# Kernel tuning notes

Measured on AMD Instinct MI355X. Metric: run time of the kernel, lower is better.

The kernel has to match this reference:

```python
import jax, jax.numpy as jnp
import numpy as np

# Forest of complete binary trees modeling query plans.
B = 512          # number of plans (trees)
D = 11           # tree depth; leaves at level D-1
LEAVES = 1 << (D - 1)      # 1024 leaves per tree
N_INT = LEAVES - 1         # 1023 internal nodes per tree (BFS heap order)
F_LEAF = 64      # leaf ('Scan') feature dim
F_INT = 32       # internal operator feature dim
H = 128          # hidden_dim
NHID = 4         # num_layers=5 -> input layer + 4 hidden layers
DV = 32          # data_vec_dim
OUT = 1 + DV     # latency + data vector


def _mlp(x, W_in, b_in, W_hid, b_hid, W_out, b_out):
    """GenericUnit: Linear+ReLU input layer, NHID Linear+ReLU hidden layers, linear output."""
    h = jax.nn.relu(x @ W_in + b_in)
    for i in range(W_hid.shape[0]):  # small fixed loop over layers
        h = jax.nn.relu(h @ W_hid[i] + b_hid[i])
    return h @ W_out + b_out


def setup_inputs() -> dict:
    key = jax.random.key(0)
    ks = jax.random.split(key, 8)

    def w(k, shape, fan_in):
        return jax.random.normal(k, shape, jnp.float32) * np.float32(1.0 / np.sqrt(fan_in))

    return {
        "leaf_feat": jax.random.normal(ks[0], (B, LEAVES, F_LEAF), jnp.float32),
        "int_feat": jax.random.normal(ks[1], (B, N_INT, F_INT), jnp.float32),
        # leaf unit (0 children)
        "leaf_W_in": w(ks[2], (F_LEAF, H), F_LEAF),
        "leaf_b_in": jnp.zeros((H,), jnp.float32),
        "leaf_W_hid": w(ks[3], (NHID, H, H), H),
        "leaf_b_hid": jnp.zeros((NHID, H), jnp.float32),
        "leaf_W_out": w(ks[4], (H, OUT), H),
        "leaf_b_out": jnp.zeros((OUT,), jnp.float32),
        # internal unit (2 children): input = F_INT + 2*OUT = 98
        "int_W_in": w(ks[5], (F_INT + 2 * OUT, H), F_INT + 2 * OUT),
        "int_b_in": jnp.zeros((H,), jnp.float32),
        "int_W_hid": w(ks[6], (NHID, H, H), H),
        "int_b_hid": jnp.zeros((NHID, H), jnp.float32),
        "int_W_out": w(ks[7], (H, OUT), H),
        "int_b_out": jnp.zeros((OUT,), jnp.float32),
    }


def reference(leaf_feat, int_feat,
              leaf_W_in, leaf_b_in, leaf_W_hid, leaf_b_hid, leaf_W_out, leaf_b_out,
              int_W_in, int_b_in, int_W_hid, int_b_hid, int_W_out, int_b_out):
    # Leaves (level D-1): [B, LEAVES, OUT]
    cur = _mlp(leaf_feat, leaf_W_in, leaf_b_in, leaf_W_hid, leaf_b_hid, leaf_W_out, leaf_b_out)
    # Bottom-up over internal levels; level d has 2^d nodes at BFS offsets [2^d-1, 2^(d+1)-1)
    for d in range(D - 2, -1, -1):
        n = 1 << d
        feats = int_feat[:, n - 1: 2 * n - 1, :]            # [B, n, F_INT]
        children = cur.reshape(B, n, 2 * OUT)               # concat of two child outputs
        unit_in = jnp.concatenate([feats, children], axis=-1)
        cur = _mlp(unit_in, int_W_in, int_b_in, int_W_hid, int_b_hid, int_W_out, int_b_out)
    # Root output, latency channel: [B]
    return cur[:, 0, 0]
```

## Files before the change

kernel.cpp:

```cpp
#include <hip/hip_runtime.h>
#include <cstdint>
#include <cstddef>

constexpr int Bn     = 512;
constexpr int Dd     = 11;
constexpr int LEAVES = 1024;
constexpr int NINT   = 1023;
constexpr int FLEAF  = 64;
constexpr int FINT   = 32;
constexpr int Hh     = 128;
constexpr int OUTC   = 33;

#define THREADS 256
constexpr int KSTR  = 136;
constexpr int MATSZ = 128 * KSTR;

using short8 = __attribute__((ext_vector_type(8))) short;
using f32x4  = __attribute__((ext_vector_type(4))) float;

__device__ __forceinline__ unsigned int f2bf_rne_u(float f) {
  unsigned int u = __float_as_uint(f);
  u += 0x7fffu + ((u >> 16) & 1);
  return u;
}
__device__ __forceinline__ unsigned short f2bf_rne(float f) {
  return (unsigned short)(f2bf_rne_u(f) >> 16);
}
__device__ __forceinline__ float bf2f(unsigned short h) {
  return __uint_as_float((unsigned int)h << 16);
}
__device__ __forceinline__ float trunc_bf(float a) {
  return __uint_as_float(__float_as_uint(a) & 0xffff0000u);
}
__device__ __forceinline__ unsigned int pack_hi_trunc(float a, float b) {
  return (__float_as_uint(a) >> 16) | (__float_as_uint(b) & 0xffff0000u);
}
__device__ __forceinline__ unsigned int pack_lo_rne(float a, float b) {
  return (f2bf_rne_u(a) >> 16) | (f2bf_rne_u(b) & 0xffff0000u);
}

template <int KC, int MT>
__device__ __forceinline__ void dense_layer(
    unsigned short* Ah, unsigned short* Al,
    const unsigned short* __restrict__ WTh, const unsigned short* __restrict__ WTl,
    const float* __restrict__ bias)
{
  const int tid  = threadIdx.x;
  const int wave = tid >> 6;
  const int lane = tid & 63;
  const int quad = lane >> 4;
  const int l16  = lane & 15;
  const int nbase = wave * 32;

  short8 wh[2][KC];
#pragma unroll
  for (int nt = 0; nt < 2; ++nt) {
    const int n = nbase + nt * 16 + l16;
#pragma unroll
    for (int kc = 0; kc < KC; ++kc)
      wh[nt][kc] = *(const short8*)&WTh[n * KSTR + kc * 32 + quad * 8];
  }
  float4 bv[2];
#pragma unroll
  for (int nt = 0; nt < 2; ++nt)
    bv[nt] = *(const float4*)&bias[nbase + nt * 16 + quad * 4];

  f32x4 c[MT][2];
#pragma unroll
  for (int mt = 0; mt < MT; ++mt)
#pragma unroll
    for (int nt = 0; nt < 2; ++nt) c[mt][nt] = (f32x4){0.f, 0.f, 0.f, 0.f};

#pragma unroll
  for (int kc = 0; kc < KC; ++kc) {
    const int k0 = kc * 32 + quad * 8;
    short8 wl[2];
#pragma unroll
    for (int nt = 0; nt < 2; ++nt) {
      const int n = nbase + nt * 16 + l16;
      wl[nt] = *(const short8*)&WTl[n * KSTR + k0];
    }
    short8 ah[MT], al[MT];
#pragma unroll
    for (int mt = 0; mt < MT; ++mt) {
      ah[mt] = *(const short8*)&Ah[(mt * 16 + l16) * KSTR + k0];
      al[mt] = *(const short8*)&Al[(mt * 16 + l16) * KSTR + k0];
    }
#pragma unroll
    for (int mt = 0; mt < MT; ++mt)
#pragma unroll
      for (int nt = 0; nt < 2; ++nt)
        c[mt][nt] = __builtin_amdgcn_mfma_f32_16x16x32_bf16(wh[nt][kc], ah[mt], c[mt][nt], 0, 0, 0);
#pragma unroll
    for (int mt = 0; mt < MT; ++mt)
#pragma unroll
      for (int nt = 0; nt < 2; ++nt)
        c[mt][nt] = __builtin_amdgcn_mfma_f32_16x16x32_bf16(wh[nt][kc], al[mt], c[mt][nt], 0, 0, 0);
#pragma unroll
    for (int mt = 0; mt < MT; ++mt)
#pragma unroll
      for (int nt = 0; nt < 2; ++nt)
        c[mt][nt] = __builtin_amdgcn_mfma_f32_16x16x32_bf16(wl[nt], ah[mt], c[mt][nt], 0, 0, 0);
  }
  __syncthreads();

#pragma unroll
  for (int mt = 0; mt < MT; ++mt) {
    const int m = mt * 16 + l16;
#pragma unroll
    for (int nt = 0; nt < 2; ++nt) {
      const int nb = nbase + nt * 16 + quad * 4;
      float v0 = fmaxf(c[mt][nt][0] + bv[nt].x, 0.f);
      float v1 = fmaxf(c[mt][nt][1] + bv[nt].y, 0.f);
      float v2 = fmaxf(c[mt][nt][2] + bv[nt].z, 0.f);
      float v3 = fmaxf(c[mt][nt][3] + bv[nt].w, 0.f);
      const unsigned int h0 = pack_hi_trunc(v0, v1);
      const unsigned int h1 = pack_hi_trunc(v2, v3);
      const unsigned int l0 = pack_lo_rne(v0 - trunc_bf(v0), v1 - trunc_bf(v1));
      const unsigned int l1 = pack_lo_rne(v2 - trunc_bf(v2), v3 - trunc_bf(v3));
      *(uint2*)&Ah[m * KSTR + nb] = make_uint2(h0, h1);
      *(uint2*)&Al[m * KSTR + nb] = make_uint2(l0, l1);
    }
  }
  __syncthreads();
}

template <int MT>
__device__ __forceinline__ void out_layer(
    const unsigned short* Ah, const unsigned short* Al,
    const unsigned short* __restrict__ WTh, const unsigned short* __restrict__ WTl,
    const float* __restrict__ bias,
    unsigned short* outH, unsigned short* outL, float* finalOut)
{
  const int tid  = threadIdx.x;
  const int wave = tid >> 6;
  const int lane = tid & 63;
  const int quad = lane >> 4;
  const int l16  = lane & 15;
  if (wave < 3) {
    const int n_row = wave * 16 + l16;
    short8 wh[4], wl[4];
#pragma unroll
    for (int kc = 0; kc < 4; ++kc) {
      wh[kc] = *(const short8*)&WTh[n_row * KSTR + kc * 32 + quad * 8];
      wl[kc] = *(const short8*)&WTl[n_row * KSTR + kc * 32 + quad * 8];
    }
    const int nb = wave * 16 + quad * 4;
    const float4 bv = *(const float4*)&bias[nb];
    const float bvr[4] = {bv.x, bv.y, bv.z, bv.w};

    f32x4 c[MT];
#pragma unroll
    for (int mt = 0; mt < MT; ++mt) c[mt] = (f32x4){0.f, 0.f, 0.f, 0.f};
#pragma unroll
    for (int kc = 0; kc < 4; ++kc) {
      const int k0 = kc * 32 + quad * 8;
#pragma unroll
      for (int mt = 0; mt < MT; ++mt) {
        const short8 ah = *(const short8*)&Ah[(mt * 16 + l16) * KSTR + k0];
        const short8 al = *(const short8*)&Al[(mt * 16 + l16) * KSTR + k0];
        c[mt] = __builtin_amdgcn_mfma_f32_16x16x32_bf16(wh[kc], ah, c[mt], 0, 0, 0);
        c[mt] = __builtin_amdgcn_mfma_f32_16x16x32_bf16(wh[kc], al, c[mt], 0, 0, 0);
        c[mt] = __builtin_amdgcn_mfma_f32_16x16x32_bf16(wl[kc], ah, c[mt], 0, 0, 0);
      }
    }
#pragma unroll
    for (int mt = 0; mt < MT; ++mt) {
      const int m = mt * 16 + l16;
#pragma unroll
      for (int r = 0; r < 4; ++r) {
        const int n = nb + r;
        const float v = c[mt][r] + bvr[r];
        if (n < OUTC) {
          outH[m * 33 + n] = (unsigned short)(__float_as_uint(v) >> 16);
          outL[m * 33 + n] = f2bf_rne(v - trunc_bf(v));
        }
        if (finalOut && n == 0 && m == 0) *finalOut = v;
      }
    }
  }
}

__global__ __launch_bounds__(THREADS, 4)
void leaf_kernel(const float* __restrict__ X,
                 const unsigned short* __restrict__ warena,
                 const float* __restrict__ barena,
                 unsigned short* __restrict__ outH, unsigned short* __restrict__ outL)
{
  __shared__ unsigned short Ah[64 * KSTR];
  __shared__ unsigned short Al[64 * KSTR];
  const int row_base = blockIdx.x * 64;
  const int tid = threadIdx.x;

  for (int e = tid; e < 64 * 16; e += THREADS) {
    const int r  = e >> 4;
    const int k0 = (e & 15) << 2;
    const float4 v = *(const float4*)&X[(size_t)(row_base + r) * FLEAF + k0];
    const unsigned int h0 = pack_hi_trunc(v.x, v.y);
    const unsigned int h1 = pack_hi_trunc(v.z, v.w);
    const unsigned int l0 = pack_lo_rne(v.x - trunc_bf(v.x), v.y - trunc_bf(v.y));
    const unsigned int l1 = pack_lo_rne(v.z - trunc_bf(v.z), v.w - trunc_bf(v.w));
    *(uint2*)&Ah[r * KSTR + k0] = make_uint2(h0, h1);
    *(uint2*)&Al[r * KSTR + k0] = make_uint2(l0, l1);
  }
  __syncthreads();

  dense_layer<2, 4>(Ah, Al, warena + 0 * 2 * MATSZ, warena + 0 * 2 * MATSZ + MATSZ, barena + 0 * 128);
#pragma unroll
  for (int l = 0; l < 4; ++l) {
    const int id = 1 + l;
    dense_layer<4, 4>(Ah, Al, warena + id * 2 * MATSZ, warena + id * 2 * MATSZ + MATSZ, barena + id * 128);
  }
  out_layer<4>(Ah, Al, warena + 5 * 2 * MATSZ, warena + 5 * 2 * MATSZ + MATSZ, barena + 5 * 128,
               outH + (size_t)row_base * 33, outL + (size_t)row_base * 33, nullptr);
}

__global__ __launch_bounds__(THREADS, 4)
void int_kernel(const float* __restrict__ feat,
                const unsigned short* __restrict__ prevH, const unsigned short* __restrict__ prevL,
                const unsigned short* __restrict__ warena, const float* __restrict__ barena,
                unsigned short* __restrict__ outH, unsigned short* __restrict__ outL,
                int n, int logn)
{
  __shared__ unsigned short Ah[64 * KSTR];
  __shared__ unsigned short Al[64 * KSTR];
  const int tid = threadIdx.x;
  const int m = tid & 63;
  const int g = tid >> 6;
  const int row = blockIdx.x * 64 + m;
  const int b = row >> logn;
  const int i = row & (n - 1);

  const float* fr = feat + ((size_t)b * NINT + (n - 1) + i) * FINT;
#pragma unroll
  for (int j = 0; j < 4; ++j) {
    const int cch = g + 4 * j;
    const float2 v = *(const float2*)&fr[cch * 2];
    *(unsigned int*)&Ah[m * KSTR + cch * 2] = pack_hi_trunc(v.x, v.y);
    *(unsigned int*)&Al[m * KSTR + cch * 2] = pack_lo_rne(v.x - trunc_bf(v.x), v.y - trunc_bf(v.y));
  }
  const size_t c0 = ((size_t)b * (n << 1) + (i << 1)) * 33;
#pragma unroll
  for (int j = 0; j < 9; ++j) {
    const int p = g + 4 * j;
    if (p < 33) {
      const unsigned int hv = *(const unsigned int*)&prevH[c0 + 2 * p];
      const unsigned int lv = *(const unsigned int*)&prevL[c0 + 2 * p];
      *(unsigned int*)&Ah[m * KSTR + 32 + 2 * p] = hv;
      *(unsigned int*)&Al[m * KSTR + 32 + 2 * p] = lv;
    }
  }
#pragma unroll
  for (int j = 0; j < 4; ++j) {
    const int p = g + 4 * j;
    if (p < 15) {
      *(unsigned int*)&Ah[m * KSTR + 98 + 2 * p] = 0u;
      *(unsigned int*)&Al[m * KSTR + 98 + 2 * p] = 0u;
    }
  }
  __syncthreads();

  dense_layer<4, 4>(Ah, Al, warena + 6 * 2 * MATSZ, warena + 6 * 2 * MATSZ + MATSZ, barena + 6 * 128);
#pragma unroll
  for (int l = 0; l < 4; ++l) {
    const int id = 7 + l;
    dense_layer<4, 4>(Ah, Al, warena + id * 2 * MATSZ, warena + id * 2 * MATSZ + MATSZ, barena + id * 128);
  }
  out_layer<4>(Ah, Al, warena + 11 * 2 * MATSZ, warena + 11 * 2 * MATSZ + MATSZ, barena + 11 * 128,
               outH + (size_t)blockIdx.x * 64 * 33, outL + (size_t)blockIdx.x * 64 * 33, nullptr);
}

__global__ __launch_bounds__(THREADS, 4)
void tail_kernel(const float* __restrict__ feat,
                 const unsigned short* __restrict__ g6H, const unsigned short* __restrict__ g6L,
                 const unsigned short* __restrict__ warena, const float* __restrict__ barena,
                 float* __restrict__ out)
{
  __shared__ unsigned short Ah[64 * KSTR];
  __shared__ unsigned short Al[64 * KSTR];
  __shared__ unsigned short oH[64 * 33];
  __shared__ unsigned short oL[64 * 33];
  const int tid = threadIdx.x;
  const int m = tid & 63;
  const int g = tid >> 6;
  const int b = blockIdx.x;

  for (int d = 5; d >= 0; --d) {
    const int n = 1 << d;
    const int i = m & (n - 1);
    const float* fr = feat + ((size_t)b * NINT + (n - 1) + i) * FINT;
#pragma unroll
    for (int j = 0; j < 4; ++j) {
      const int cch = g + 4 * j;
      const float2 v = *(const float2*)&fr[cch * 2];
      *(unsigned int*)&Ah[m * KSTR + cch * 2] = pack_hi_trunc(v.x, v.y);
      *(unsigned int*)&Al[m * KSTR + cch * 2] = pack_lo_rne(v.x - trunc_bf(v.x), v.y - trunc_bf(v.y));
    }
    const unsigned short* sH;
    const unsigned short* sL;
    size_t c0;
    if (d == 5) { sH = g6H; sL = g6L; c0 = ((size_t)b * 64 + 2 * i) * 33; }
    else        { sH = oH;  sL = oL;  c0 = (size_t)(2 * i) * 33; }
#pragma unroll
    for (int j = 0; j < 9; ++j) {
      const int p = g + 4 * j;
      if (p < 33) {
        const unsigned int hv = *(const unsigned int*)&sH[c0 + 2 * p];
        const unsigned int lv = *(const unsigned int*)&sL[c0 + 2 * p];
        *(unsigned int*)&Ah[m * KSTR + 32 + 2 * p] = hv;
        *(unsigned int*)&Al[m * KSTR + 32 + 2 * p] = lv;
      }
    }
#pragma unroll
    for (int j = 0; j < 4; ++j) {
      const int p = g + 4 * j;
      if (p < 15) {
        *(unsigned int*)&Ah[m * KSTR + 98 + 2 * p] = 0u;
        *(unsigned int*)&Al[m * KSTR + 98 + 2 * p] = 0u;
      }
    }
    __syncthreads();

    if (d == 5) {
      dense_layer<4, 2>(Ah, Al, warena + 6 * 2 * MATSZ, warena + 6 * 2 * MATSZ + MATSZ, barena + 6 * 128);
#pragma unroll
      for (int l = 0; l < 4; ++l) {
        const int id = 7 + l;
        dense_layer<4, 2>(Ah, Al, warena + id * 2 * MATSZ, warena + id * 2 * MATSZ + MATSZ, barena + id * 128);
      }
      out_layer<2>(Ah, Al, warena + 11 * 2 * MATSZ, warena + 11 * 2 * MATSZ + MATSZ, barena + 11 * 128,
                   oH, oL, nullptr);
    } else {
      dense_layer<4, 1>(Ah, Al, warena + 6 * 2 * MATSZ, warena + 6 * 2 * MATSZ + MATSZ, barena + 6 * 128);
#pragma unroll
      for (int l = 0; l < 4; ++l) {
        const int id = 7 + l;
        dense_layer<4, 1>(Ah, Al, warena + id * 2 * MATSZ, warena + id * 2 * MATSZ + MATSZ, barena + id * 128);
      }
      out_layer<1>(Ah, Al, warena + 11 * 2 * MATSZ, warena + 11 * 2 * MATSZ + MATSZ, barena + 11 * 128,
                   oH, oL, (d == 0) ? (out + b) : nullptr);
    }
    __syncthreads();
  }
}

__global__ void prep_kernel(const float* __restrict__ lW_in, const float* __restrict__ lW_hid,
                            const float* __restrict__ lW_out, const float* __restrict__ lb_in,
                            const float* __restrict__ lb_hid, const float* __restrict__ lb_out,
                            const float* __restrict__ iW_in, const float* __restrict__ iW_hid,
                            const float* __restrict__ iW_out, const float* __restrict__ ib_in,
                            const float* __restrict__ ib_hid, const float* __restrict__ ib_out,
                            unsigned short* __restrict__ warena, float* __restrict__ barena)
{
  const int id = blockIdx.y;
  const float* W; const float* bs; int K, N;
  if (id == 0)       { W = lW_in;                        bs = lb_in;                 K = FLEAF; N = Hh; }
  else if (id <= 4)  { W = lW_hid + (id - 1) * Hh * Hh;  bs = lb_hid + (id - 1) * Hh; K = Hh;   N = Hh; }
  else if (id == 5)  { W = lW_out;                       bs = lb_out;                K = Hh;    N = OUTC; }
  else if (id == 6)  { W = iW_in;                        bs = ib_in;                 K = FINT + 2 * OUTC; N = Hh; }
  else if (id <= 10) { W = iW_hid + (id - 7) * Hh * Hh;  bs = ib_hid + (id - 7) * Hh; K = Hh;   N = Hh; }
  else               { W = iW_out;                       bs = ib_out;                K = Hh;    N = OUTC; }

  unsigned short* dh = warena + id * 2 * MATSZ;
  unsigned short* dl = dh + MATSZ;
  const int e = blockIdx.x * THREADS + threadIdx.x;
  if (e < MATSZ) {
    const int nn = e / KSTR;
    const int kk = e - nn * KSTR;
    const float v = (kk < K && nn < N) ? W[(size_t)kk * N + nn] : 0.f;
    const unsigned short h = f2bf_rne(v);
    dh[e] = h;
    dl[e] = f2bf_rne(v - bf2f(h));
  }
  if (blockIdx.x == 0 && threadIdx.x < 128)
    barena[id * 128 + threadIdx.x] = (threadIdx.x < N) ? bs[threadIdx.x] : 0.f;
}

extern "C" void kernel_launch(void* const* d_in, const int* in_sizes, int n_in,
                              void* d_out, int out_size, void* d_ws, size_t ws_size,
                              hipStream_t stream) {
  const float* leaf_feat = (const float*)d_in[0];
  const float* int_feat  = (const float*)d_in[1];
  const float* lW_in  = (const float*)d_in[2];
  const float* lb_in  = (const float*)d_in[3];
  const float* lW_hid = (const float*)d_in[4];
  const float* lb_hid = (const float*)d_in[5];
  const float* lW_out = (const float*)d_in[6];
  const float* lb_out = (const float*)d_in[7];
  const float* iW_in  = (const float*)d_in[8];
  const float* ib_in  = (const float*)d_in[9];
  const float* iW_hid = (const float*)d_in[10];
  const float* ib_hid = (const float*)d_in[11];
  const float* iW_out = (const float*)d_in[12];
  const float* ib_out = (const float*)d_in[13];
  float* out = (float*)d_out;

  const size_t rowsA = (size_t)Bn * LEAVES;
  const size_t rowsB = rowsA / 2;
  unsigned short* AH = (unsigned short*)d_ws;
  unsigned short* AL = AH + rowsA * 33;
  unsigned short* BH = AL + rowsA * 33;
  unsigned short* BL = BH + rowsB * 33;
  unsigned short* warena = BL + rowsB * 33;
  float* barena = (float*)(warena + 24 * MATSZ);

  prep_kernel<<<dim3((MATSZ + THREADS - 1) / THREADS, 12), THREADS, 0, stream>>>(
      lW_in, lW_hid, lW_out, lb_in, lb_hid, lb_out,
      iW_in, iW_hid, iW_out, ib_in, ib_hid, ib_out, warena, barena);

  leaf_kernel<<<(Bn * LEAVES) / 64, THREADS, 0, stream>>>(leaf_feat, warena, barena, AH, AL);

  int_kernel<<<4096, THREADS, 0, stream>>>(int_feat, AH, AL, warena, barena, BH, BL, 512, 9);
  int_kernel<<<2048, THREADS, 0, stream>>>(int_feat, BH, BL, warena, barena, AH, AL, 256, 8);
  int_kernel<<<1024, THREADS, 0, stream>>>(int_feat, AH, AL, warena, barena, BH, BL, 128, 7);
  int_kernel<<< 512, THREADS, 0, stream>>>(int_feat, BH, BL, warena, barena, AH, AL,  64, 6);

  tail_kernel<<<Bn, THREADS, 0, stream>>>(int_feat, AH, AL, warena, barena, out);
}
```

Before: 930.7 us.

## Preload low weights, double-buffer LDS activation reads, coalesce int-kernel input staging

The dense and output layers now load all low-part weight fragments into registers up front and double-buffer the high-part activation fragments from LDS, so the next k-chunk's reads overlap the current MFMAs, with s_setprio raised around the MFMA blocks. The int kernel's staging of features and child outputs is reorganised into contiguous, coalesced float4 and uint loads across the whole block instead of per-row strided reads. The low-part bf16 packing uses the hardware v_cvt_pk_bf16_f32 instruction. Launch-bounds occupancy drops from 4 to 3 blocks per CU to make room for the extra registers, which may reduce latency hiding.

```diff
diff --git a/kernel.cpp b/kernel.cpp
--- a/kernel.cpp
+++ b/kernel.cpp
@@ -36,7 +36,9 @@
   return (__float_as_uint(a) >> 16) | (__float_as_uint(b) & 0xffff0000u);
 }
 __device__ __forceinline__ unsigned int pack_lo_rne(float a, float b) {
-  return (f2bf_rne_u(a) >> 16) | (f2bf_rne_u(b) & 0xffff0000u);
+  unsigned int r;
+  asm("v_cvt_pk_bf16_f32 %0, %1, %2" : "=v"(r) : "v"(a), "v"(b));
+  return r;
 }
 
 template <int KC, int MT>
@@ -52,57 +54,66 @@
   const int l16  = lane & 15;
   const int nbase = wave * 32;
 
-  short8 wh[2][KC];
+  short8 wh[2][KC], wl[2][KC];
 #pragma unroll
   for (int nt = 0; nt < 2; ++nt) {
     const int n = nbase + nt * 16 + l16;
 #pragma unroll
-    for (int kc = 0; kc < KC; ++kc)
+    for (int kc = 0; kc < KC; ++kc) {
       wh[nt][kc] = *(const short8*)&WTh[n * KSTR + kc * 32 + quad * 8];
-  }
+      wl[nt][kc] = *(const short8*)&WTl[n * KSTR + kc * 32 + quad * 8];
+    }
+  }
+
+  f32x4 c[MT][2];
+#pragma unroll
+  for (int mt = 0; mt < MT; ++mt)
+#pragma unroll
+    for (int nt = 0; nt < 2; ++nt) c[mt][nt] = (f32x4){0.f, 0.f, 0.f, 0.f};
+
+  short8 ah[2][MT];
+  short8 al[MT];
+#pragma unroll
+  for (int mt = 0; mt < MT; ++mt)
+    ah[0][mt] = *(const short8*)&Ah[(mt * 16 + l16) * KSTR + quad * 8];
+
+#pragma unroll
+  for (int kc = 0; kc < KC; ++kc) {
+    const int cur = kc & 1;
+    const int k0  = kc * 32 + quad * 8;
+#pragma unroll
+    for (int mt = 0; mt < MT; ++mt)
+      al[mt] = *(const short8*)&Al[(mt * 16 + l16) * KSTR + k0];
+    if (kc + 1 < KC) {
+      const int k1 = k0 + 32;
+#pragma unroll
+      for (int mt = 0; mt < MT; ++mt)
+        ah[cur ^ 1][mt] = *(const short8*)&Ah[(mt * 16 + l16) * KSTR + k1];
+    }
+    __builtin_amdgcn_s_setprio(1);
+#pragma unroll
+    for (int mt = 0; mt < MT; ++mt)
+#pragma unroll
+      for (int nt = 0; nt < 2; ++nt)
+        c[mt][nt] = __builtin_amdgcn_mfma_f32_16x16x32_bf16(wh[nt][kc], ah[cur][mt], c[mt][nt], 0, 0, 0);
+#pragma unroll
+    for (int mt = 0; mt < MT; ++mt)
+#pragma unroll
+      for (int nt = 0; nt < 2; ++nt)
+        c[mt][nt] = __builtin_amdgcn_mfma_f32_16x16x32_bf16(wl[nt][kc], ah[cur][mt], c[mt][nt], 0, 0, 0);
+#pragma unroll
+    for (int mt = 0; mt < MT; ++mt)
+#pragma unroll
+      for (int nt = 0; nt < 2; ++nt)
+        c[mt][nt] = __builtin_amdgcn_mfma_f32_16x16x32_bf16(wh[nt][kc], al[mt], c[mt][nt], 0, 0, 0);
+    __builtin_amdgcn_s_setprio(0);
+  }
+  __syncthreads();
+
   float4 bv[2];
 #pragma unroll
   for (int nt = 0; nt < 2; ++nt)
     bv[nt] = *(const float4*)&bias[nbase + nt * 16 + quad * 4];
-
-  f32x4 c[MT][2];
-#pragma unroll
-  for (int mt = 0; mt < MT; ++mt)
-#pragma unroll
-    for (int nt = 0; nt < 2; ++nt) c[mt][nt] = (f32x4){0.f, 0.f, 0.f, 0.f};
-
-#pragma unroll
-  for (int kc = 0; kc < KC; ++kc) {
-    const int k0 = kc * 32 + quad * 8;
-    short8 wl[2];
-#pragma unroll
-    for (int nt = 0; nt < 2; ++nt) {
-      const int n = nbase + nt * 16 + l16;
-      wl[nt] = *(const short8*)&WTl[n * KSTR + k0];
-    }
-    short8 ah[MT], al[MT];
-#pragma unroll
-    for (int mt = 0; mt < MT; ++mt) {
-      ah[mt] = *(const short8*)&Ah[(mt * 16 + l16) * KSTR + k0];
-      al[mt] = *(const short8*)&Al[(mt * 16 + l16) * KSTR + k0];
-    }
-#pragma unroll
-    for (int mt = 0; mt < MT; ++mt)
-#pragma unroll
-      for (int nt = 0; nt < 2; ++nt)
-        c[mt][nt] = __builtin_amdgcn_mfma_f32_16x16x32_bf16(wh[nt][kc], ah[mt], c[mt][nt], 0, 0, 0);
-#pragma unroll
-    for (int mt = 0; mt < MT; ++mt)
-#pragma unroll
-      for (int nt = 0; nt < 2; ++nt)
-        c[mt][nt] = __builtin_amdgcn_mfma_f32_16x16x32_bf16(wh[nt][kc], al[mt], c[mt][nt], 0, 0, 0);
-#pragma unroll
-    for (int mt = 0; mt < MT; ++mt)
-#pragma unroll
-      for (int nt = 0; nt < 2; ++nt)
-        c[mt][nt] = __builtin_amdgcn_mfma_f32_16x16x32_bf16(wl[nt], ah[mt], c[mt][nt], 0, 0, 0);
-  }
-  __syncthreads();
 
 #pragma unroll
   for (int mt = 0; mt < MT; ++mt) {
@@ -152,17 +163,34 @@
     f32x4 c[MT];
 #pragma unroll
     for (int mt = 0; mt < MT; ++mt) c[mt] = (f32x4){0.f, 0.f, 0.f, 0.f};
+
+    short8 ah[2][MT];
+    short8 al[MT];
+#pragma unroll
+    for (int mt = 0; mt < MT; ++mt)
+      ah[0][mt] = *(const short8*)&Ah[(mt * 16 + l16) * KSTR + quad * 8];
+
 #pragma unroll
     for (int kc = 0; kc < 4; ++kc) {
-      const int k0 = kc * 32 + quad * 8;
+      const int cur = kc & 1;
+      const int k0  = kc * 32 + quad * 8;
+#pragma unroll
+      for (int mt = 0; mt < MT; ++mt)
+        al[mt] = *(const short8*)&Al[(mt * 16 + l16) * KSTR + k0];
+      if (kc + 1 < 4) {
+        const int k1 = k0 + 32;
+#pragma unroll
+        for (int mt = 0; mt < MT; ++mt)
+          ah[cur ^ 1][mt] = *(const short8*)&Ah[(mt * 16 + l16) * KSTR + k1];
+      }
+      __builtin_amdgcn_s_setprio(1);
 #pragma unroll
       for (int mt = 0; mt < MT; ++mt) {
-        const short8 ah = *(const short8*)&Ah[(mt * 16 + l16) * KSTR + k0];
-        const short8 al = *(const short8*)&Al[(mt * 16 + l16) * KSTR + k0];
-        c[mt] = __builtin_amdgcn_mfma_f32_16x16x32_bf16(wh[kc], ah, c[mt], 0, 0, 0);
-        c[mt] = __builtin_amdgcn_mfma_f32_16x16x32_bf16(wh[kc], al, c[mt], 0, 0, 0);
-        c[mt] = __builtin_amdgcn_mfma_f32_16x16x32_bf16(wl[kc], ah, c[mt], 0, 0, 0);
-      }
+        c[mt] = __builtin_amdgcn_mfma_f32_16x16x32_bf16(wh[kc], ah[cur][mt], c[mt], 0, 0, 0);
+        c[mt] = __builtin_amdgcn_mfma_f32_16x16x32_bf16(wl[kc], ah[cur][mt], c[mt], 0, 0, 0);
+        c[mt] = __builtin_amdgcn_mfma_f32_16x16x32_bf16(wh[kc], al[mt], c[mt], 0, 0, 0);
+      }
+      __builtin_amdgcn_s_setprio(0);
     }
 #pragma unroll
     for (int mt = 0; mt < MT; ++mt) {
@@ -181,7 +209,7 @@
   }
 }
 
-__global__ __launch_bounds__(THREADS, 4)
+__global__ __launch_bounds__(THREADS, 3)
 void leaf_kernel(const float* __restrict__ X,
                  const unsigned short* __restrict__ warena,
                  const float* __restrict__ barena,
@@ -215,7 +243,7 @@
                outH + (size_t)row_base * 33, outL + (size_t)row_base * 33, nullptr);
 }
 
-__global__ __launch_bounds__(THREADS, 4)
+__global__ __launch_bounds__(THREADS, 3)
 void int_kernel(const float* __restrict__ feat,
                 const unsigned short* __restrict__ prevH, const unsigned short* __restrict__ prevL,
                 const unsigned short* __restrict__ warena, const float* __restrict__ barena,
@@ -224,32 +252,40 @@
 {
   __shared__ unsigned short Ah[64 * KSTR];
   __shared__ unsigned short Al[64 * KSTR];
-  const int tid = threadIdx.x;
+  const int tid  = threadIdx.x;
+  const int row0 = blockIdx.x * 64;
+  const int b    = row0 >> logn;
+  const int i0   = row0 & (n - 1);
+
+  const float* fr0 = feat + ((size_t)b * NINT + (n - 1) + i0) * FINT;
+#pragma unroll
+  for (int j = 0; j < 2; ++j) {
+    const int e  = tid + j * 256;
+    const int r  = e >> 3;
+    const int cc = (e & 7) << 2;
+    const float4 v = *(const float4*)&fr0[(size_t)e << 2];
+    const unsigned int h0 = pack_hi_trunc(v.x, v.y);
+    const unsigned int h1 = pack_hi_trunc(v.z, v.w);
+    const unsigned int l0 = pack_lo_rne(v.x - trunc_bf(v.x), v.y - trunc_bf(v.y));
+    const unsigned int l1 = pack_lo_rne(v.z - trunc_bf(v.z), v.w - trunc_bf(v.w));
+    *(uint2*)&Ah[r * KSTR + cc] = make_uint2(h0, h1);
+    *(uint2*)&Al[r * KSTR + cc] = make_uint2(l0, l1);
+  }
+  const size_t cbase = ((size_t)b * (n << 1) + (size_t)(i0 << 1)) * 33;
+  const unsigned int* srcH = (const unsigned int*)(prevH + cbase);
+  const unsigned int* srcL = (const unsigned int*)(prevL + cbase);
+#pragma unroll
+  for (int j = 0; j < 9; ++j) {
+    const int idx = tid + j * 256;
+    if (idx < 2112) {
+      const unsigned int mm = (unsigned int)idx / 33u;
+      const unsigned int pp = (unsigned int)idx - mm * 33u;
+      *(unsigned int*)&Ah[mm * KSTR + 32 + 2 * pp] = srcH[idx];
+      *(unsigned int*)&Al[mm * KSTR + 32 + 2 * pp] = srcL[idx];
+    }
+  }
   const int m = tid & 63;
   const int g = tid >> 6;
-  const int row = blockIdx.x * 64 + m;
-  const int b = row >> logn;
-  const int i = row & (n - 1);
-
-  const float* fr = feat + ((size_t)b * NINT + (n - 1) + i) * FINT;
-#pragma unroll
-  for (int j = 0; j < 4; ++j) {
-    const int cch = g + 4 * j;
-    const float2 v = *(const float2*)&fr[cch * 2];
-    *(unsigned int*)&Ah[m * KSTR + cch * 2] = pack_hi_trunc(v.x, v.y);
-    *(unsigned int*)&Al[m * KSTR + cch * 2] = pack_lo_rne(v.x - trunc_bf(v.x), v.y - trunc_bf(v.y));
-  }
-  const size_t c0 = ((size_t)b * (n << 1) + (i << 1)) * 33;
-#pragma unroll
-  for (int j = 0; j < 9; ++j) {
-    const int p = g + 4 * j;
-    if (p < 33) {
-      const unsigned int hv = *(const unsigned int*)&prevH[c0 + 2 * p];
-      const unsigned int lv = *(const unsigned int*)&prevL[c0 + 2 * p];
-      *(unsigned int*)&Ah[m * KSTR + 32 + 2 * p] = hv;
-      *(unsigned int*)&Al[m * KSTR + 32 + 2 * p] = lv;
-    }
-  }
 #pragma unroll
   for (int j = 0; j < 4; ++j) {
     const int p = g + 4 * j;
@@ -270,7 +306,7 @@
                outH + (size_t)blockIdx.x * 64 * 33, outL + (size_t)blockIdx.x * 64 * 33, nullptr);
 }
 
-__global__ __launch_bounds__(THREADS, 4)
+__global__ __launch_bounds__(THREADS, 3)
 void tail_kernel(const float* __restrict__ feat,
                  const unsigned short* __restrict__ g6H, const unsigned short* __restrict__ g6L,
                  const unsigned short* __restrict__ warena, const float* __restrict__ barena,
```

Measured after the change: 973.7 us. +4.6%, slower.

## Replace fused tail kernel with per-level int_kernel launches and hardware bf16 pack

Applied to the files above, without the earlier changes.

Removes the tail kernel, which had one block per tree walk levels 5..0 in sequence with rows padded to 16 or 32. Those six levels now go through the same int_kernel launched once per level with row-dense 64-row blocks. The root latency is written from the last launch through a per-row finalOut pointer. The low-half bf16 pack now uses the v_cvt_pk_bf16_f32 instruction instead of manual round-to-nearest-even bit arithmetic. In exchange the top levels need six extra small launches, and the smallest grids leave most CUs idle.

```diff
diff --git a/kernel.cpp b/kernel.cpp
--- a/kernel.cpp
+++ b/kernel.cpp
@@ -36,7 +36,9 @@
   return (__float_as_uint(a) >> 16) | (__float_as_uint(b) & 0xffff0000u);
 }
 __device__ __forceinline__ unsigned int pack_lo_rne(float a, float b) {
-  return (f2bf_rne_u(a) >> 16) | (f2bf_rne_u(b) & 0xffff0000u);
+  unsigned int r;
+  asm("v_cvt_pk_bf16_f32 %0, %1, %2" : "=v"(r) : "v"(a), "v"(b));
+  return r;
 }
 
 template <int KC, int MT>
@@ -175,7 +177,7 @@
           outH[m * 33 + n] = (unsigned short)(__float_as_uint(v) >> 16);
           outL[m * 33 + n] = f2bf_rne(v - trunc_bf(v));
         }
-        if (finalOut && n == 0 && m == 0) *finalOut = v;
+        if (finalOut && n == 0) finalOut[m] = v;
       }
     }
   }
@@ -220,6 +222,7 @@
                 const unsigned short* __restrict__ prevH, const unsigned short* __restrict__ prevL,
                 const unsigned short* __restrict__ warena, const float* __restrict__ barena,
                 unsigned short* __restrict__ outH, unsigned short* __restrict__ outL,
+                float* __restrict__ finalOut,
                 int n, int logn)
 {
   __shared__ unsigned short Ah[64 * KSTR];
@@ -267,81 +270,8 @@
     dense_layer<4, 4>(Ah, Al, warena + id * 2 * MATSZ, warena + id * 2 * MATSZ + MATSZ, barena + id * 128);
   }
   out_layer<4>(Ah, Al, warena + 11 * 2 * MATSZ, warena + 11 * 2 * MATSZ + MATSZ, barena + 11 * 128,
-               outH + (size_t)blockIdx.x * 64 * 33, outL + (size_t)blockIdx.x * 64 * 33, nullptr);
-}
-
-__global__ __launch_bounds__(THREADS, 4)
-void tail_kernel(const float* __restrict__ feat,
-                 const unsigned short* __restrict__ g6H, const unsigned short* __restrict__ g6L,
-                 const unsigned short* __restrict__ warena, const float* __restrict__ barena,
-                 float* __restrict__ out)
-{
-  __shared__ unsigned short Ah[64 * KSTR];
-  __shared__ unsigned short Al[64 * KSTR];
-  __shared__ unsigned short oH[64 * 33];
-  __shared__ unsigned short oL[64 * 33];
-  const int tid = threadIdx.x;
-  const int m = tid & 63;
-  const int g = tid >> 6;
-  const int b = blockIdx.x;
-
-  for (int d = 5; d >= 0; --d) {
-    const int n = 1 << d;
-    const int i = m & (n - 1);
-    const float* fr = feat + ((size_t)b * NINT + (n - 1) + i) * FINT;
-#pragma unroll
-    for (int j = 0; j < 4; ++j) {
-      const int cch = g + 4 * j;
-      const float2 v = *(const float2*)&fr[cch * 2];
-      *(unsigned int*)&Ah[m * KSTR + cch * 2] = pack_hi_trunc(v.x, v.y);
-      *(unsigned int*)&Al[m * KSTR + cch * 2] = pack_lo_rne(v.x - trunc_bf(v.x), v.y - trunc_bf(v.y));
-    }
-    const unsigned short* sH;
-    const unsigned short* sL;
-    size_t c0;
-    if (d == 5) { sH = g6H; sL = g6L; c0 = ((size_t)b * 64 + 2 * i) * 33; }
-    else        { sH = oH;  sL = oL;  c0 = (size_t)(2 * i) * 33; }
-#pragma unroll
-    for (int j = 0; j < 9; ++j) {
-      const int p = g + 4 * j;
-      if (p < 33) {
-        const unsigned int hv = *(const unsigned int*)&sH[c0 + 2 * p];
-        const unsigned int lv = *(const unsigned int*)&sL[c0 + 2 * p];
-        *(unsigned int*)&Ah[m * KSTR + 32 + 2 * p] = hv;
-        *(unsigned int*)&Al[m * KSTR + 32 + 2 * p] = lv;
-      }
-    }
-#pragma unroll
-    for (int j = 0; j < 4; ++j) {
-      const int p = g + 4 * j;
-      if (p < 15) {
-        *(unsigned int*)&Ah[m * KSTR + 98 + 2 * p] = 0u;
-        *(unsigned int*)&Al[m * KSTR + 98 + 2 * p] = 0u;
-      }
-    }
-    __syncthreads();
-
-    if (d == 5) {
-      dense_layer<4, 2>(Ah, Al, warena + 6 * 2 * MATSZ, warena + 6 * 2 * MATSZ + MATSZ, barena + 6 * 128);
-#pragma unroll
-      for (int l = 0; l < 4; ++l) {
-        const int id = 7 + l;
-        dense_layer<4, 2>(Ah, Al, warena + id * 2 * MATSZ, warena + id * 2 * MATSZ + MATSZ, barena + id * 128);
-      }
-      out_layer<2>(Ah, Al, warena + 11 * 2 * MATSZ, warena + 11 * 2 * MATSZ + MATSZ, barena + 11 * 128,
-                   oH, oL, nullptr);
-    } else {
-      dense_layer<4, 1>(Ah, Al, warena + 6 * 2 * MATSZ, warena + 6 * 2 * MATSZ + MATSZ, barena + 6 * 128);
-#pragma unroll
-      for (int l = 0; l < 4; ++l) {
-        const int id = 7 + l;
-        dense_layer<4, 1>(Ah, Al, warena + id * 2 * MATSZ, warena + id * 2 * MATSZ + MATSZ, barena + id * 128);
-      }
-      out_layer<1>(Ah, Al, warena + 11 * 2 * MATSZ, warena + 11 * 2 * MATSZ + MATSZ, barena + 11 * 128,
-                   oH, oL, (d == 0) ? (out + b) : nullptr);
-    }
-    __syncthreads();
-  }
+               outH + (size_t)blockIdx.x * 64 * 33, outL + (size_t)blockIdx.x * 64 * 33,
+               finalOut ? (finalOut + blockIdx.x * 64) : nullptr);
 }
 
 __global__ void prep_kernel(const float* __restrict__ lW_in, const float* __restrict__ lW_hid,
@@ -410,10 +340,14 @@
 
   leaf_kernel<<<(Bn * LEAVES) / 64, THREADS, 0, stream>>>(leaf_feat, warena, barena, AH, AL);
 
-  int_kernel<<<4096, THREADS, 0, stream>>>(int_feat, AH, AL, warena, barena, BH, BL, 512, 9);
-  int_kernel<<<2048, THREADS, 0, stream>>>(int_feat, BH, BL, warena, barena, AH, AL, 256, 8);
-  int_kernel<<<1024, THREADS, 0, stream>>>(int_feat, AH, AL, warena, barena, BH, BL, 128, 7);
-  int_kernel<<< 512, THREADS, 0, stream>>>(int_feat, BH, BL, warena, barena, AH, AL,  64, 6);
-
-  tail_kernel<<<Bn, THREADS, 0, stream>>>(int_feat, AH, AL, warena, barena, out);
-}
+  int_kernel<<<4096, THREADS, 0, stream>>>(int_feat, AH, AL, warena, barena, BH, BL, nullptr, 512, 9);
+  int_kernel<<<2048, THREADS, 0, stream>>>(int_feat, BH, BL, warena, barena, AH, AL, nullptr, 256, 8);
+  int_kernel<<<1024, THREADS, 0, stream>>>(int_feat, AH, AL, warena, barena, BH, BL, nullptr, 128, 7);
+  int_kernel<<< 512, THREADS, 0, stream>>>(int_feat, BH, BL, warena, barena, AH, AL, nullptr,  64, 6);
+  int_kernel<<< 256, THREADS, 0, stream>>>(int_feat, AH, AL, warena, barena, BH, BL, nullptr,  32, 5);
+  int_kernel<<< 128, THREADS, 0, stream>>>(int_feat, BH, BL, warena, barena, AH, AL, nullptr,  16, 4);
+  int_kernel<<<  64, THREADS, 0, stream>>>(int_feat, AH, AL, warena, barena, BH, BL, nullptr,   8, 3);
+  int_kernel<<<  32, THREADS, 0, stream>>>(int_feat, BH, BL, warena, barena, AH, AL, nullptr,   4, 2);
+  int_kernel<<<  16, THREADS, 0, stream>>>(int_feat, AH, AL, warena, barena, BH, BL, nullptr,   2, 1);
+  int_kernel<<<   8, THREADS, 0, stream>>>(int_feat, BH, BL, warena, barena, AH, AL, out,        1, 0);
+}
```

Measured after the change: 903.8 us. 1.03x faster.
